# Kernel tuning notes

Measured on AMD Instinct MI355X. Metric: run time of the kernel, lower is better.

## Reference

```python
import jax, jax.numpy as jnp
import numpy as np

D = 512   # word_dim
H = 4     # heads
NEG = -1.0e9


def setup_inputs() -> dict:
    key = jax.random.key(0)
    ks = jax.random.split(key, 9)
    B, N, K = 4, 1024, 32
    neibor_embedding = jax.random.normal(ks[0], (B, N, K, D), dtype=jnp.float32)
    x = jax.random.normal(ks[1], (B, N, D), dtype=jnp.float32)
    mask = jax.random.randint(ks[2], (B, N, K), 0, 2, dtype=jnp.int32)
    s = 1.0 / np.sqrt(D)
    Wq = jax.random.normal(ks[3], (D, D), dtype=jnp.float32) * s
    bq = jax.random.normal(ks[4], (D,), dtype=jnp.float32) * s
    Wk = jax.random.normal(ks[5], (D, D), dtype=jnp.float32) * s
    bk = jax.random.normal(ks[6], (D,), dtype=jnp.float32) * s
    Wv = jax.random.normal(ks[7], (D, D), dtype=jnp.float32) * s
    bv = jax.random.normal(ks[8], (D,), dtype=jnp.float32) * s
    return {"neibor_embedding": neibor_embedding, "mask": mask, "x": x,
            "Wq": Wq, "bq": bq, "Wk": Wk, "bk": bk, "Wv": Wv, "bv": bv}


def reference(neibor_embedding, mask, x, Wq, bq, Wk, bk, Wv, bv):
    B, N, K, Dm = neibor_embedding.shape
    dh = Dm // H
    # torch Linear: y = x @ W.T + b
    q = x @ Wq.T + bq                        # [B, N, D]
    k = neibor_embedding @ Wk.T + bk         # [B, N, K, D]
    v = neibor_embedding @ Wv.T + bv         # [B, N, K, D]
    q = q.reshape(B, N, H, dh)
    k = k.reshape(B, N, K, H, dh)
    v = v.reshape(B, N, K, H, dh)
    # broadcast q*k sum over head_dim -> scores [B, N, H, K] (no 1/sqrt(d) scaling, per source)
    scores = jnp.einsum('bnhd,bnkhd->bnhk', q, k)
    m = (mask[:, :, None, :] == 0)           # [B, N, 1, K] broadcasts over heads
    scores = jnp.where(m, NEG, scores)
    attn = jax.nn.softmax(scores, axis=3)    # [B, N, H, K]
    vec = jnp.einsum('bnhk,bnkhd->bnhd', attn, v)  # [B, N, H, dh]
    return vec.reshape(B, N, Dm)
```

## Files before the change

kernel.cpp:

```cpp
#include <hip/hip_runtime.h>

#define DD   512
#define KK_N 32
#define HH   4
#define DH   128
#define BN_TOT 4096

template<bool BT, int BM, int BN, int TM, int TN>
__global__ __launch_bounds__(256)
void sgemm(const float* __restrict__ A, int lda, int batchA,
           const float* __restrict__ B, int ldb, int batchB,
           float* __restrict__ C, int ldc, int batchC,
           const float* __restrict__ bias, int batchBias,
           int Kd)
{
    constexpr int BK = 16;
    constexpr int KG = BK / 4;
    constexpr int A_LOADS = (BM * BK) / (4 * 256);
    constexpr int B_LOADS = (BN * BK) / (4 * 256);
    constexpr int NTX = BN / TN;

    const int bz = blockIdx.z;
    A += (long)bz * batchA;
    B += (long)bz * batchB;
    C += (long)bz * batchC;
    if (bias) bias += (long)bz * batchBias;

    __shared__ __align__(16) float As[BK][BM + 4];
    __shared__ __align__(16) float Bs[BK][BN + 4];

    const int t  = threadIdx.x;
    const int tx = t % NTX;
    const int ty = t / NTX;
    const int rbase = blockIdx.y * BM;
    const int obase = blockIdx.x * BN;

    float acc[TM][TN] = {};

    for (int k0 = 0; k0 < Kd; k0 += BK) {
        float4 av[A_LOADS], bv[B_LOADS];
#pragma unroll
        for (int i = 0; i < A_LOADS; i++) {
            int s = t + i * 256;
            int row = s / KG, kg = s % KG;
            av[i] = *(const float4*)&A[(long)(rbase + row) * lda + k0 + kg * 4];
        }
#pragma unroll
        for (int i = 0; i < B_LOADS; i++) {
            int s = t + i * 256;
            if (BT) {
                int row = s / KG, kg = s % KG;
                bv[i] = *(const float4*)&B[(long)(obase + row) * ldb + k0 + kg * 4];
            } else {
                int kr = s / (BN / 4), oc = s % (BN / 4);
                bv[i] = *(const float4*)&B[(long)(k0 + kr) * ldb + obase + oc * 4];
            }
        }
        __syncthreads();
#pragma unroll
        for (int i = 0; i < A_LOADS; i++) {
            int s = t + i * 256;
            int row = s / KG, kg = s % KG;
            const float* ap = (const float*)&av[i];
#pragma unroll
            for (int j = 0; j < 4; j++) As[kg * 4 + j][row] = ap[j];
        }
#pragma unroll
        for (int i = 0; i < B_LOADS; i++) {
            int s = t + i * 256;
            if (BT) {
                int row = s / KG, kg = s % KG;
                const float* bp = (const float*)&bv[i];
#pragma unroll
                for (int j = 0; j < 4; j++) Bs[kg * 4 + j][row] = bp[j];
            } else {
                int kr = s / (BN / 4), oc = s % (BN / 4);
                *(float4*)&Bs[kr][oc * 4] = bv[i];
            }
        }
        __syncthreads();
#pragma unroll
        for (int kk = 0; kk < BK; kk++) {
            float a[TM], b[TN];
#pragma unroll
            for (int im = 0; im < TM / 4; im++) {
                float4 v = *(const float4*)&As[kk][ty * TM + im * 4];
                a[im*4+0] = v.x; a[im*4+1] = v.y; a[im*4+2] = v.z; a[im*4+3] = v.w;
            }
#pragma unroll
            for (int in = 0; in < TN / 4; in++) {
                float4 v = *(const float4*)&Bs[kk][tx * TN + in * 4];
                b[in*4+0] = v.x; b[in*4+1] = v.y; b[in*4+2] = v.z; b[in*4+3] = v.w;
            }
#pragma unroll
            for (int i = 0; i < TM; i++)
#pragma unroll
                for (int j = 0; j < TN; j++)
                    acc[i][j] = fmaf(a[i], b[j], acc[i][j]);
        }
    }

    float bb[TN];
#pragma unroll
    for (int j = 0; j < TN; j++) bb[j] = 0.f;
    if (bias) {
#pragma unroll
        for (int in = 0; in < TN / 4; in++) {
            float4 v = *(const float4*)&bias[obase + tx * TN + in * 4];
            bb[in*4+0] = v.x; bb[in*4+1] = v.y; bb[in*4+2] = v.z; bb[in*4+3] = v.w;
        }
    }
#pragma unroll
    for (int i = 0; i < TM; i++) {
#pragma unroll
        for (int in = 0; in < TN / 4; in++) {
            float4 o;
            o.x = acc[i][in*4+0] + bb[in*4+0];
            o.y = acc[i][in*4+1] + bb[in*4+1];
            o.z = acc[i][in*4+2] + bb[in*4+2];
            o.w = acc[i][in*4+3] + bb[in*4+3];
            *(float4*)&C[(long)(rbase + ty * TM + i) * ldc + obase + tx * TN + in * 4] = o;
        }
    }
}

__global__ __launch_bounds__(256)
void attn_fused(const float* __restrict__ ne,
                const int*   __restrict__ mask,
                const float* __restrict__ q,
                const float* g,
                const float* __restrict__ bk,
                float* wne)
{
    const int bn   = blockIdx.x;
    const int t    = threadIdx.x;
    const int wave = t >> 6;
    const int lane = t & 63;

    __shared__ __align__(16) float ne_s[16][516];
    __shared__ __align__(16) float g_s[HH * DD];
    __shared__ float part[4][16][HH];
    __shared__ float p_s[HH][16];
    __shared__ float c_s[HH];
    __shared__ float m_s[HH], l_s[HH], alpha_s[HH];

    {
        const float4* gs = (const float4*)(g + (long)bn * (HH * DD));
        float4 v0 = gs[t];
        float4 v1 = gs[t + 256];
        *(float4*)&g_s[t * 4]         = v0;
        *(float4*)&g_s[(t + 256) * 4] = v1;
    }
    {
        float2 q2 = *(const float2*)&q[(long)bn * DD + wave * DH + lane * 2];
        float2 b2 = *(const float2*)&bk[wave * DH + lane * 2];
        float cp = q2.x * b2.x + q2.y * b2.y;
#pragma unroll
        for (int off = 32; off >= 1; off >>= 1)
            cp += __shfl_xor(cp, off, 64);
        if (lane == 0) c_s[wave] = cp;
    }
    if (t < HH) { m_s[t] = -__builtin_inff(); l_s[t] = 0.f; }

    float wacc[8] = {};
    const int h_own = t >> 6;
    const int d8    = (t & 63) * 8;
    const int kk    = t & 15;
    const int rep   = t >> 4;

    for (int ch = 0; ch < 2; ch++) {
        __syncthreads();
        {
            const float4* src = (const float4*)(ne + (long)bn * (KK_N * DD) + ch * (16 * DD));
#pragma unroll
            for (int i = 0; i < 8; i++) {
                int f = i * 256 + t;
                float4 v = src[f];
                *(float4*)&ne_s[f >> 7][(f & 127) * 4] = v;
            }
        }
        __syncthreads();
        {
            float acc[HH] = {};
#pragma unroll
            for (int i = 0; i < 8; i++) {
                float4 nv = *(const float4*)&ne_s[kk][rep * 32 + i * 4];
#pragma unroll
                for (int h = 0; h < HH; h++) {
                    float4 gv = *(const float4*)&g_s[h * DD + rep * 32 + i * 4];
                    acc[h] = fmaf(nv.x, gv.x, acc[h]);
                    acc[h] = fmaf(nv.y, gv.y, acc[h]);
                    acc[h] = fmaf(nv.z, gv.z, acc[h]);
                    acc[h] = fmaf(nv.w, gv.w, acc[h]);
                }
            }
#pragma unroll
            for (int h = 0; h < HH; h++) {
                acc[h] += __shfl_xor(acc[h], 16, 64);
                acc[h] += __shfl_xor(acc[h], 32, 64);
            }
            if ((t & 48) == 0) {
#pragma unroll
                for (int h = 0; h < HH; h++) part[wave][kk][h] = acc[h];
            }
        }
        __syncthreads();
        if (t < 64) {
            int k_i = t & 15, h = t >> 4;
            float s = part[0][k_i][h] + part[1][k_i][h] + part[2][k_i][h]
                    + part[3][k_i][h] + c_s[h];
            if (mask[(long)bn * KK_N + ch * 16 + k_i] == 0) s = -1.0e9f;
            float mx = s;
#pragma unroll
            for (int off = 8; off >= 1; off >>= 1)
                mx = fmaxf(mx, __shfl_xor(mx, off, 64));
            float m_old = m_s[h];
            float m_new = fmaxf(m_old, mx);
            float p = expf(s - m_new);
            float sm = p;
#pragma unroll
            for (int off = 8; off >= 1; off >>= 1)
                sm += __shfl_xor(sm, off, 64);
            p_s[h][k_i] = p;
            if (k_i == 0) {
                float alpha = expf(m_old - m_new);
                alpha_s[h] = alpha;
                l_s[h] = l_s[h] * alpha + sm;
                m_s[h] = m_new;
            }
        }
        __syncthreads();
        {
            float alpha = alpha_s[h_own];
#pragma unroll
            for (int j = 0; j < 8; j++) wacc[j] *= alpha;
#pragma unroll
            for (int k2 = 0; k2 < 16; k2++) {
                float pk = p_s[h_own][k2];
                float4 n0 = *(const float4*)&ne_s[k2][d8];
                float4 n1 = *(const float4*)&ne_s[k2][d8 + 4];
                wacc[0] = fmaf(pk, n0.x, wacc[0]);
                wacc[1] = fmaf(pk, n0.y, wacc[1]);
                wacc[2] = fmaf(pk, n0.z, wacc[2]);
                wacc[3] = fmaf(pk, n0.w, wacc[3]);
                wacc[4] = fmaf(pk, n1.x, wacc[4]);
                wacc[5] = fmaf(pk, n1.y, wacc[5]);
                wacc[6] = fmaf(pk, n1.z, wacc[6]);
                wacc[7] = fmaf(pk, n1.w, wacc[7]);
            }
        }
    }
    float rl = 1.0f / l_s[h_own];
    float4 o0 = make_float4(wacc[0] * rl, wacc[1] * rl, wacc[2] * rl, wacc[3] * rl);
    float4 o1 = make_float4(wacc[4] * rl, wacc[5] * rl, wacc[6] * rl, wacc[7] * rl);
    float* dst = wne + (long)bn * (HH * DD) + t * 8;
    *(float4*)&dst[0] = o0;
    *(float4*)&dst[4] = o1;
}

extern "C" void kernel_launch(void* const* d_in, const int* in_sizes, int n_in,
                              void* d_out, int out_size, void* d_ws, size_t ws_size,
                              hipStream_t stream) {
    (void)in_sizes; (void)n_in; (void)out_size; (void)ws_size;
    const float* ne  = (const float*)d_in[0];
    const int*   msk = (const int*)  d_in[1];
    const float* x   = (const float*)d_in[2];
    const float* Wq  = (const float*)d_in[3];
    const float* bq  = (const float*)d_in[4];
    const float* Wk  = (const float*)d_in[5];
    const float* bk  = (const float*)d_in[6];
    const float* Wv  = (const float*)d_in[7];
    const float* bv  = (const float*)d_in[8];
    float* out = (float*)d_out;

    float* q_ws = (float*)d_ws;
    float* g_ws = q_ws + (long)BN_TOT * DD;

    dim3 blk(256);
    sgemm<true, 128, 64, 8, 4><<<dim3(8, 32, 1), blk, 0, stream>>>(
        x, DD, 0, Wq, DD, 0, q_ws, DD, 0, bq, 0, DD);
    sgemm<false, 128, 128, 8, 8><<<dim3(4, 32, HH), blk, 0, stream>>>(
        q_ws, DD, DH, Wk, DD, DH * DD, g_ws, HH * DD, DD, nullptr, 0, DH);
    attn_fused<<<dim3(BN_TOT), blk, 0, stream>>>(ne, msk, q_ws, g_ws, bk, g_ws);
    sgemm<true, 64, 128, 4, 8><<<dim3(1, 64, HH), blk, 0, stream>>>(
        g_ws, HH * DD, DD, Wv, DD, DH * DD, out, DD, DH, bv, DH, DD);
}
```

Before: 530.4 us.

## Split-K the Q and output projections and register-prefetch GEMM tiles

The Q projection and the final V projection now split their reduction dimension in two across extra grid z-slices. Each slice writes a partial result, and a new add2_bias kernel sums the two halves and adds the bias. The change also prefetches the next K-tile into registers before the inner compute loop, so global loads overlap with FMAs. In exchange it needs extra workspace, two more launches and extra memory traffic for the partial buffers; the aim is more blocks on the small GEMMs to raise occupancy.

Result: faster. 489.1 us (-7.8%).

```diff
diff --git a/kernel.cpp b/kernel.cpp
--- a/kernel.cpp
+++ b/kernel.cpp
@@ -6,12 +6,11 @@
 #define DH   128
 #define BN_TOT 4096
 
-template<bool BT, int BM, int BN, int TM, int TN>
+template<bool BT, int BM, int BN, int TM, int TN, int ZBITS>
 __global__ __launch_bounds__(256)
-void sgemm(const float* __restrict__ A, int lda, int batchA,
-           const float* __restrict__ B, int ldb, int batchB,
-           float* __restrict__ C, int ldc, int batchC,
-           const float* __restrict__ bias, int batchBias,
+void sgemm(const float* __restrict__ A, int lda, int bA1, int bA0,
+           const float* __restrict__ B, int ldb, int bB1, int bB0,
+           float* __restrict__ C, int ldc, int bC1, int bC0,
            int Kd)
 {
     constexpr int BK = 16;
@@ -20,11 +19,11 @@
     constexpr int B_LOADS = (BN * BK) / (4 * 256);
     constexpr int NTX = BN / TN;
 
-    const int bz = blockIdx.z;
-    A += (long)bz * batchA;
-    B += (long)bz * batchB;
-    C += (long)bz * batchC;
-    if (bias) bias += (long)bz * batchBias;
+    const int zlo = blockIdx.z & ((1 << ZBITS) - 1);
+    const int zhi = blockIdx.z >> ZBITS;
+    A += (long)zhi * bA1 + (long)zlo * bA0;
+    B += (long)zhi * bB1 + (long)zlo * bB0;
+    C += (long)zhi * bC1 + (long)zlo * bC0;
 
     __shared__ __align__(16) float As[BK][BM + 4];
     __shared__ __align__(16) float Bs[BK][BN + 4];
@@ -35,14 +34,11 @@
     const int rbase = blockIdx.y * BM;
     const int obase = blockIdx.x * BN;
 
-    float acc[TM][TN] = {};
-
-    for (int k0 = 0; k0 < Kd; k0 += BK) {
-        float4 av[A_LOADS], bv[B_LOADS];
+    float4 av[A_LOADS], bv[B_LOADS];
+    auto loadAB = [&](int k0) {
 #pragma unroll
         for (int i = 0; i < A_LOADS; i++) {
-            int s = t + i * 256;
-            int row = s / KG, kg = s % KG;
+            int s = t + i * 256, row = s / KG, kg = s % KG;
             av[i] = *(const float4*)&A[(long)(rbase + row) * lda + k0 + kg * 4];
         }
 #pragma unroll
@@ -56,11 +52,16 @@
                 bv[i] = *(const float4*)&B[(long)(k0 + kr) * ldb + obase + oc * 4];
             }
         }
+    };
+
+    float acc[TM][TN] = {};
+    loadAB(0);
+
+    for (int k0 = 0; k0 < Kd; k0 += BK) {
         __syncthreads();
 #pragma unroll
         for (int i = 0; i < A_LOADS; i++) {
-            int s = t + i * 256;
-            int row = s / KG, kg = s % KG;
+            int s = t + i * 256, row = s / KG, kg = s % KG;
             const float* ap = (const float*)&av[i];
 #pragma unroll
             for (int j = 0; j < 4; j++) As[kg * 4 + j][row] = ap[j];
@@ -79,6 +80,7 @@
             }
         }
         __syncthreads();
+        if (k0 + BK < Kd) loadAB(k0 + BK);
 #pragma unroll
         for (int kk = 0; kk < BK; kk++) {
             float a[TM], b[TN];
@@ -100,27 +102,32 @@
         }
     }
 
-    float bb[TN];
-#pragma unroll
-    for (int j = 0; j < TN; j++) bb[j] = 0.f;
-    if (bias) {
-#pragma unroll
-        for (int in = 0; in < TN / 4; in++) {
-            float4 v = *(const float4*)&bias[obase + tx * TN + in * 4];
-            bb[in*4+0] = v.x; bb[in*4+1] = v.y; bb[in*4+2] = v.z; bb[in*4+3] = v.w;
-        }
-    }
 #pragma unroll
     for (int i = 0; i < TM; i++) {
 #pragma unroll
         for (int in = 0; in < TN / 4; in++) {
             float4 o;
-            o.x = acc[i][in*4+0] + bb[in*4+0];
-            o.y = acc[i][in*4+1] + bb[in*4+1];
-            o.z = acc[i][in*4+2] + bb[in*4+2];
-            o.w = acc[i][in*4+3] + bb[in*4+3];
+            o.x = acc[i][in*4+0];
+            o.y = acc[i][in*4+1];
+            o.z = acc[i][in*4+2];
+            o.w = acc[i][in*4+3];
             *(float4*)&C[(long)(rbase + ty * TM + i) * ldc + obase + tx * TN + in * 4] = o;
         }
+    }
+}
+
+__global__ __launch_bounds__(256)
+void add2_bias(const float4* __restrict__ a, const float4* __restrict__ b,
+               const float4* __restrict__ bias, float4* __restrict__ o, int n4)
+{
+    for (int i = blockIdx.x * 256 + threadIdx.x; i < n4; i += gridDim.x * 256) {
+        float4 va = a[i], vb = b[i], vc = bias[i & 127];
+        float4 r;
+        r.x = va.x + vb.x + vc.x;
+        r.y = va.y + vb.y + vc.y;
+        r.z = va.z + vb.z + vc.z;
+        r.w = va.w + vb.w + vc.w;
+        o[i] = r;
     }
 }
 
@@ -273,15 +280,24 @@
     const float* bv  = (const float*)d_in[8];
     float* out = (float*)d_out;
 
-    float* q_ws = (float*)d_ws;
-    float* g_ws = q_ws + (long)BN_TOT * DD;
+    const long NQ = (long)BN_TOT * DD;
+    float* q_ws  = (float*)d_ws;
+    float* g_ws  = q_ws + NQ;
+    float* qpart = g_ws + (long)BN_TOT * HH * DD;
+    float* opart = qpart + 2 * NQ;
 
     dim3 blk(256);
-    sgemm<true, 128, 64, 8, 4><<<dim3(8, 32, 1), blk, 0, stream>>>(
-        x, DD, 0, Wq, DD, 0, q_ws, DD, 0, bq, 0, DD);
-    sgemm<false, 128, 128, 8, 8><<<dim3(4, 32, HH), blk, 0, stream>>>(
-        q_ws, DD, DH, Wk, DD, DH * DD, g_ws, HH * DD, DD, nullptr, 0, DH);
+    sgemm<true, 128, 64, 8, 4, 1><<<dim3(8, 32, 2), blk, 0, stream>>>(
+        x, DD, 0, 256, Wq, DD, 0, 256, qpart, DD, 0, (int)NQ, 256);
+    add2_bias<<<dim3(512), blk, 0, stream>>>(
+        (const float4*)qpart, (const float4*)(qpart + NQ),
+        (const float4*)bq, (float4*)q_ws, (int)(NQ / 4));
+    sgemm<false, 128, 128, 8, 8, 0><<<dim3(4, 32, HH), blk, 0, stream>>>(
+        q_ws, DD, DH, 0, Wk, DD, DH * DD, 0, g_ws, HH * DD, DD, 0, DH);
     attn_fused<<<dim3(BN_TOT), blk, 0, stream>>>(ne, msk, q_ws, g_ws, bk, g_ws);
-    sgemm<true, 64, 128, 4, 8><<<dim3(1, 64, HH), blk, 0, stream>>>(
-        g_ws, HH * DD, DD, Wv, DD, DH * DD, out, DD, DH, bv, DH, DD);
+    sgemm<true, 128, 64, 8, 4, 1><<<dim3(2, 32, 2 * HH), blk, 0, stream>>>(
+        g_ws, HH * DD, DD, 256, Wv, DD, DH * DD, 256, opart, DD, DH, (int)NQ, 256);
+    add2_bias<<<dim3(512), blk, 0, stream>>>(
+        (const float4*)opart, (const float4*)(opart + NQ),
+        (const float4*)bv, (float4*)out, (int)(NQ / 4));
 }
```
